# Optimization experiments

Hardware: AMD Instinct MI355X
Metric: run time of the kernel (lower is better)

Reference implementation:

```python
import jax, jax.numpy as jnp
import numpy as np

N_NODES = 50000
N_EDGES = 600000
IN_DIM = 128
HID = 128
OUT_DIM = 2


def _init_linear(key, out_dim, in_dim):
    scale = 1.0 / np.sqrt(in_dim)
    return jax.random.uniform(key, (out_dim, in_dim), jnp.float32, -scale, scale)


def setup_inputs() -> dict:
    key = jax.random.key(0)
    ks = jax.random.split(key, 12)
    x = jax.random.normal(ks[0], (N_NODES, IN_DIM), jnp.float32)
    edge_index = jax.random.randint(ks[1], (2, N_EDGES), 0, N_NODES, jnp.int64)
    dims = [(HID, IN_DIM), (HID, HID), (OUT_DIM, HID)]
    inp = {"x": x, "edge_index": edge_index}
    for i, (o, d) in enumerate(dims):
        inp[f"Wl{i}"] = _init_linear(ks[2 + 3 * i], o, d)      # lin_l: applied to aggregated neighbors
        inp[f"Wr{i}"] = _init_linear(ks[3 + 3 * i], o, d)      # lin_r: applied to root (self) features
        inp[f"b{i}"] = jnp.zeros((o,), jnp.float32)            # bias of lin_l
    return inp


def _sage_conv(x, src, dst, Wl, Wr, b):
    # mean-aggregate source features onto target nodes, then linear transform
    msgs = x[src]                                              # [E, d] gather
    agg = jax.ops.segment_sum(msgs, dst, num_segments=N_NODES)
    cnt = jax.ops.segment_sum(jnp.ones((src.shape[0], 1), x.dtype), dst,
                              num_segments=N_NODES)
    agg = agg / jnp.maximum(cnt, 1.0)                          # mean over in-edges
    return agg @ Wl.T + b + x @ Wr.T


def reference(x, edge_index, Wl0, Wr0, b0, Wl1, Wr1, b1, Wl2, Wr2, b2):
    src, dst = edge_index[0], edge_index[1]
    # eval mode: dropout is identity
    h = jax.nn.relu(_sage_conv(x, src, dst, Wl0, Wr0, b0))
    h = jax.nn.relu(_sage_conv(h, src, dst, Wl1, Wr1, b1))
    return _sage_conv(h, src, dst, Wl2, Wr2, b2)
```

## Files before the change

kernel.cpp:

```cpp
#include <hip/hip_runtime.h>
#include <hip/hip_bf16.h>

#define N_NODES 50000
#define N_EDGES 600000
#define DIM 128
#define CAP 64

typedef short bf16x8 __attribute__((ext_vector_type(8)));
typedef float f32x4 __attribute__((ext_vector_type(4)));

__device__ __forceinline__ ushort f2b(float f) {
    __hip_bfloat16 h = __float2bfloat16(f);
    return *reinterpret_cast<ushort*>(&h);
}
__device__ __forceinline__ float b2f_lo(unsigned u) { return __uint_as_float(u << 16); }
__device__ __forceinline__ float b2f_hi(unsigned u) { return __uint_as_float(u & 0xffff0000u); }

static constexpr size_t alignup(size_t x) { return (x + 255) & ~size_t(255); }
static constexpr size_t OFF_FLAG = 0;
static constexpr size_t OFF_CNT  = 256;
static constexpr size_t OFF_COL  = alignup(OFF_CNT + sizeof(unsigned) * N_NODES);
static constexpr size_t OFF_XBF  = alignup(OFF_COL + sizeof(int) * (size_t)N_NODES * CAP);
static constexpr size_t OFF_AGG  = alignup(OFF_XBF + sizeof(ushort) * N_NODES * DIM);
static constexpr size_t OFF_H1   = alignup(OFF_AGG + sizeof(ushort) * N_NODES * DIM);
static constexpr size_t OFF_Z    = alignup(OFF_H1 + sizeof(ushort) * N_NODES * DIM);
static constexpr size_t OFF_RT   = alignup(OFF_Z + sizeof(float) * 2 * N_NODES);
static constexpr size_t OFF_WL0  = alignup(OFF_RT + sizeof(float) * 2 * N_NODES);
static constexpr size_t OFF_WR0  = alignup(OFF_WL0 + sizeof(ushort) * DIM * DIM);
static constexpr size_t OFF_WL1  = alignup(OFF_WR0 + sizeof(ushort) * DIM * DIM);
static constexpr size_t OFF_WR1  = alignup(OFF_WL1 + sizeof(ushort) * DIM * DIM);

__global__ __launch_bounds__(256) void prep_k(const int* __restrict__ ei,
                                              const float* __restrict__ x,
                                              const float* __restrict__ wa, const float* __restrict__ wb,
                                              const float* __restrict__ wc, const float* __restrict__ wd,
                                              unsigned* __restrict__ flag,
                                              unsigned* __restrict__ cnt,
                                              ushort* __restrict__ xbf,
                                              ushort* __restrict__ oa, ushort* __restrict__ ob,
                                              ushort* __restrict__ oc, ushort* __restrict__ od) {
    const int bid = blockIdx.x, t = threadIdx.x;
    if (bid < 6250) {
        const int i = bid * 256 + t;
        float4 v = reinterpret_cast<const float4*>(x)[i];
        ushort4 o;
        o.x = f2b(v.x); o.y = f2b(v.y); o.z = f2b(v.z); o.w = f2b(v.w);
        reinterpret_cast<ushort4*>(xbf)[i] = o;
        if (i < N_NODES) cnt[i] = 0u;
        if (bid == 0) {
            __shared__ unsigned any;
            if (t == 0) any = 0u;
            __syncthreads();
            unsigned hv = 0;
#pragma unroll
            for (int j = 0; j < 4; ++j) hv |= (unsigned)ei[2 * (t * 4 + j) + 1];
            if (hv) atomicOr(&any, 1u);
            __syncthreads();
            if (t == 0) *flag = any;
        }
    } else {
        const int wb_i = bid - 6250;
        const int w = wb_i >> 4;
        const float* src = (w == 0) ? wa : (w == 1) ? wb : (w == 2) ? wc : wd;
        ushort* dst      = (w == 0) ? oa : (w == 1) ? ob : (w == 2) ? oc : od;
        const int i = (wb_i & 15) * 256 + t;
        float4 v = reinterpret_cast<const float4*>(src)[i];
        ushort4 o;
        o.x = f2b(v.x); o.y = f2b(v.y); o.z = f2b(v.z); o.w = f2b(v.w);
        reinterpret_cast<ushort4*>(dst)[i] = o;
    }
}

__global__ void fillcsr_k(const int* __restrict__ ei, const unsigned* __restrict__ flag,
                          unsigned* __restrict__ cnt, int* __restrict__ col) {
    int e0 = (blockIdx.x * 256 + threadIdx.x) * 4;
    if (e0 >= N_EDGES) return;
    int s[4], d[4];
    if (*flag) {
        uint4 sv = *reinterpret_cast<const uint4*>(&ei[e0]);
        uint4 dv = *reinterpret_cast<const uint4*>(&ei[N_EDGES + e0]);
        s[0] = sv.x; s[1] = sv.y; s[2] = sv.z; s[3] = sv.w;
        d[0] = dv.x; d[1] = dv.y; d[2] = dv.z; d[3] = dv.w;
    } else {
        uint4 sa = *reinterpret_cast<const uint4*>(&ei[2 * e0]);
        uint4 sb = *reinterpret_cast<const uint4*>(&ei[2 * e0 + 4]);
        uint4 da = *reinterpret_cast<const uint4*>(&ei[2 * (N_EDGES + e0)]);
        uint4 db = *reinterpret_cast<const uint4*>(&ei[2 * (N_EDGES + e0) + 4]);
        s[0] = sa.x; s[1] = sa.z; s[2] = sb.x; s[3] = sb.z;
        d[0] = da.x; d[1] = da.z; d[2] = db.x; d[3] = db.z;
    }
#pragma unroll
    for (int i = 0; i < 4; ++i) {
        unsigned pos = atomicAdd(&cnt[d[i]], 1u);
        if (pos < CAP) col[(size_t)d[i] * CAP + pos] = s[i];
    }
}

__global__ __launch_bounds__(256) void agg_k(const ushort* __restrict__ h,
                                             const unsigned* __restrict__ cnt,
                                             const int* __restrict__ col,
                                             ushort* __restrict__ aggm) {
    const int g = threadIdx.x >> 4, lane = threadIdx.x & 15;
    const int node = blockIdx.x * 16 + g;
    if (node >= N_NODES) return;
    unsigned deg = cnt[node];
    if (deg > CAP) deg = CAP;
    const int* cp = &col[(size_t)node * CAP];
    float acc[8];
#pragma unroll
    for (int i = 0; i < 8; ++i) acc[i] = 0.f;
    const int co = lane * 8;
    unsigned e = 0;
    for (; e + 4 <= deg; e += 4) {
        const int s0 = cp[e], s1 = cp[e + 1], s2 = cp[e + 2], s3 = cp[e + 3];
        const uint4 v0 = *reinterpret_cast<const uint4*>(&h[(size_t)s0 * DIM + co]);
        const uint4 v1 = *reinterpret_cast<const uint4*>(&h[(size_t)s1 * DIM + co]);
        const uint4 v2 = *reinterpret_cast<const uint4*>(&h[(size_t)s2 * DIM + co]);
        const uint4 v3 = *reinterpret_cast<const uint4*>(&h[(size_t)s3 * DIM + co]);
        acc[0] += b2f_lo(v0.x) + b2f_lo(v1.x) + b2f_lo(v2.x) + b2f_lo(v3.x);
        acc[1] += b2f_hi(v0.x) + b2f_hi(v1.x) + b2f_hi(v2.x) + b2f_hi(v3.x);
        acc[2] += b2f_lo(v0.y) + b2f_lo(v1.y) + b2f_lo(v2.y) + b2f_lo(v3.y);
        acc[3] += b2f_hi(v0.y) + b2f_hi(v1.y) + b2f_hi(v2.y) + b2f_hi(v3.y);
        acc[4] += b2f_lo(v0.z) + b2f_lo(v1.z) + b2f_lo(v2.z) + b2f_lo(v3.z);
        acc[5] += b2f_hi(v0.z) + b2f_hi(v1.z) + b2f_hi(v2.z) + b2f_hi(v3.z);
        acc[6] += b2f_lo(v0.w) + b2f_lo(v1.w) + b2f_lo(v2.w) + b2f_lo(v3.w);
        acc[7] += b2f_hi(v0.w) + b2f_hi(v1.w) + b2f_hi(v2.w) + b2f_hi(v3.w);
    }
    for (; e < deg; ++e) {
        const int s = cp[e];
        const uint4 v = *reinterpret_cast<const uint4*>(&h[(size_t)s * DIM + co]);
        acc[0] += b2f_lo(v.x); acc[1] += b2f_hi(v.x);
        acc[2] += b2f_lo(v.y); acc[3] += b2f_hi(v.y);
        acc[4] += b2f_lo(v.z); acc[5] += b2f_hi(v.z);
        acc[6] += b2f_lo(v.w); acc[7] += b2f_hi(v.w);
    }
    const float inv = 1.0f / fmaxf((float)deg, 1.0f);
    uint4 o;
    o.x = (unsigned)f2b(acc[0] * inv) | ((unsigned)f2b(acc[1] * inv) << 16);
    o.y = (unsigned)f2b(acc[2] * inv) | ((unsigned)f2b(acc[3] * inv) << 16);
    o.z = (unsigned)f2b(acc[4] * inv) | ((unsigned)f2b(acc[5] * inv) << 16);
    o.w = (unsigned)f2b(acc[6] * inv) | ((unsigned)f2b(acc[7] * inv) << 16);
    *reinterpret_cast<uint4*>(&aggm[(size_t)node * DIM + co]) = o;
}

__global__ __launch_bounds__(256) void xform_mfma_k(const ushort* __restrict__ A0,
                                                    const ushort* __restrict__ A1,
                                                    const ushort* __restrict__ Wl,
                                                    const ushort* __restrict__ Wr,
                                                    const float*  __restrict__ bias,
                                                    ushort* __restrict__ hout) {
    __shared__ ushort Ws[128 * 136];
    const int t    = threadIdx.x;
    const int wave = t >> 6;
    const int l    = t & 63;
    const int l16  = l & 15;
    const int lk   = (l >> 4) * 8;
    const int node = blockIdx.x * 64 + wave * 16 + l16;
    const bool valid = node < N_NODES;

    const int wrow = t >> 1;
    const int wc0  = (t & 1) * 64;

    f32x4 acc[8];
#pragma unroll
    for (int i = 0; i < 8; ++i) acc[i] = (f32x4){0.f, 0.f, 0.f, 0.f};

    const bf16x8 zfrag = (bf16x8){0, 0, 0, 0, 0, 0, 0, 0};

#pragma unroll
    for (int p = 0; p < 2; ++p) {
        const ushort* Asrc = p ? A1 : A0;
        const ushort* Wsrc = p ? Wr : Wl;

        bf16x8 bf[4];
#pragma unroll
        for (int ks = 0; ks < 4; ++ks)
            bf[ks] = valid
                ? *reinterpret_cast<const bf16x8*>(&Asrc[(size_t)node * DIM + ks * 32 + lk])
                : zfrag;

        __syncthreads();
        {
            const uint4* src = reinterpret_cast<const uint4*>(&Wsrc[(size_t)wrow * DIM + wc0]);
            uint4* dst = reinterpret_cast<uint4*>(&Ws[wrow * 136 + wc0]);
#pragma unroll
            for (int i = 0; i < 8; ++i) dst[i] = src[i];
        }
        __syncthreads();

#pragma unroll
        for (int ks = 0; ks < 4; ++ks) {
            const int kb = ks * 32;
#pragma unroll
            for (int ot = 0; ot < 8; ++ot) {
                const bf16x8 afrag = *reinterpret_cast<const bf16x8*>(
                    &Ws[(ot * 16 + l16) * 136 + kb + lk]);
                acc[ot] = __builtin_amdgcn_mfma_f32_16x16x32_bf16(afrag, bf[ks], acc[ot], 0, 0, 0);
            }
        }
    }

    if (!valid) return;
    const int orow = (l >> 4) * 4;
#pragma unroll
    for (int ot = 0; ot < 8; ++ot) {
        const float4 b4 = *reinterpret_cast<const float4*>(&bias[ot * 16 + orow]);
        float r0 = fmaxf(acc[ot][0] + b4.x, 0.f);
        float r1 = fmaxf(acc[ot][1] + b4.y, 0.f);
        float r2 = fmaxf(acc[ot][2] + b4.z, 0.f);
        float r3 = fmaxf(acc[ot][3] + b4.w, 0.f);
        ushort4 s;
        s.x = f2b(r0); s.y = f2b(r1); s.z = f2b(r2); s.w = f2b(r3);
        *reinterpret_cast<ushort4*>(&hout[(size_t)node * DIM + ot * 16 + orow]) = s;
    }
}

__global__ __launch_bounds__(256) void xform_final_k(const ushort* __restrict__ A0,
                                                     const ushort* __restrict__ A1,
                                                     const ushort* __restrict__ Wl,
                                                     const ushort* __restrict__ Wr,
                                                     const float*  __restrict__ bias,
                                                     const float*  __restrict__ Wl2,
                                                     const float*  __restrict__ Wr2,
                                                     const float*  __restrict__ b2,
                                                     float* __restrict__ z,
                                                     float* __restrict__ rt) {
    __shared__ ushort Ws[128 * 136];
    __shared__ float wl2s[256], wr2s[256];
    const int t    = threadIdx.x;
    const int wave = t >> 6;
    const int l    = t & 63;
    const int l16  = l & 15;
    const int lk   = (l >> 4) * 8;
    const int node = blockIdx.x * 64 + wave * 16 + l16;
    const bool valid = node < N_NODES;

    const int wrow = t >> 1;
    const int wc0  = (t & 1) * 64;

    wl2s[t] = Wl2[t];
    wr2s[t] = Wr2[t];

    f32x4 acc[8];
#pragma unroll
    for (int i = 0; i < 8; ++i) acc[i] = (f32x4){0.f, 0.f, 0.f, 0.f};

    const bf16x8 zfrag = (bf16x8){0, 0, 0, 0, 0, 0, 0, 0};

#pragma unroll
    for (int p = 0; p < 2; ++p) {
        const ushort* Asrc = p ? A1 : A0;
        const ushort* Wsrc = p ? Wr : Wl;

        bf16x8 bf[4];
#pragma unroll
        for (int ks = 0; ks < 4; ++ks)
            bf[ks] = valid
                ? *reinterpret_cast<const bf16x8*>(&Asrc[(size_t)node * DIM + ks * 32 + lk])
                : zfrag;

        __syncthreads();
        {
            const uint4* src = reinterpret_cast<const uint4*>(&Wsrc[(size_t)wrow * DIM + wc0]);
            uint4* dst = reinterpret_cast<uint4*>(&Ws[wrow * 136 + wc0]);
#pragma unroll
            for (int i = 0; i < 8; ++i) dst[i] = src[i];
        }
        __syncthreads();

#pragma unroll
        for (int ks = 0; ks < 4; ++ks) {
            const int kb = ks * 32;
#pragma unroll
            for (int ot = 0; ot < 8; ++ot) {
                const bf16x8 afrag = *reinterpret_cast<const bf16x8*>(
                    &Ws[(ot * 16 + l16) * 136 + kb + lk]);
                acc[ot] = __builtin_amdgcn_mfma_f32_16x16x32_bf16(afrag, bf[ks], acc[ot], 0, 0, 0);
            }
        }
    }

    const int orow = (l >> 4) * 4;
    float z0 = 0.f, z1 = 0.f, r0s = 0.f, r1s = 0.f;
#pragma unroll
    for (int ot = 0; ot < 8; ++ot) {
        const int o = ot * 16 + orow;
        const float4 b4 = *reinterpret_cast<const float4*>(&bias[o]);
        const float h0 = fmaxf(acc[ot][0] + b4.x, 0.f);
        const float h1v = fmaxf(acc[ot][1] + b4.y, 0.f);
        const float h2v = fmaxf(acc[ot][2] + b4.z, 0.f);
        const float h3 = fmaxf(acc[ot][3] + b4.w, 0.f);
        z0  += h0 * wl2s[o] + h1v * wl2s[o + 1] + h2v * wl2s[o + 2] + h3 * wl2s[o + 3];
        z1  += h0 * wl2s[128 + o] + h1v * wl2s[128 + o + 1] + h2v * wl2s[128 + o + 2] + h3 * wl2s[128 + o + 3];
        r0s += h0 * wr2s[o] + h1v * wr2s[o + 1] + h2v * wr2s[o + 2] + h3 * wr2s[o + 3];
        r1s += h0 * wr2s[128 + o] + h1v * wr2s[128 + o + 1] + h2v * wr2s[128 + o + 2] + h3 * wr2s[128 + o + 3];
    }
    z0  += __shfl_xor(z0, 16);  z0  += __shfl_xor(z0, 32);
    z1  += __shfl_xor(z1, 16);  z1  += __shfl_xor(z1, 32);
    r0s += __shfl_xor(r0s, 16); r0s += __shfl_xor(r0s, 32);
    r1s += __shfl_xor(r1s, 16); r1s += __shfl_xor(r1s, 32);
    if ((l >> 4) == 0 && valid) {
        float2 zv = {z0, z1};
        float2 rv = {r0s + b2[0], r1s + b2[1]};
        *reinterpret_cast<float2*>(&z[(size_t)node * 2])  = zv;
        *reinterpret_cast<float2*>(&rt[(size_t)node * 2]) = rv;
    }
}

__global__ __launch_bounds__(256) void outgather_k(const float* __restrict__ z,
                                                   const float* __restrict__ rt,
                                                   const unsigned* __restrict__ cnt,
                                                   const int* __restrict__ col,
                                                   float* __restrict__ out) {
    const int g = threadIdx.x >> 3, lane = threadIdx.x & 7;
    const int node = blockIdx.x * 32 + g;
    if (node >= N_NODES) return;
    unsigned deg = cnt[node];
    if (deg > CAP) deg = CAP;
    const int* cp = &col[(size_t)node * CAP];
    float s0 = 0.f, s1 = 0.f;
    for (unsigned e = lane; e < deg; e += 8) {
        const int s = cp[e];
        const float2 v = *reinterpret_cast<const float2*>(&z[(size_t)s * 2]);
        s0 += v.x; s1 += v.y;
    }
#pragma unroll
    for (int m = 1; m < 8; m <<= 1) {
        s0 += __shfl_xor(s0, m);
        s1 += __shfl_xor(s1, m);
    }
    if (lane == 0) {
        const float inv = 1.0f / fmaxf((float)deg, 1.0f);
        const float2 rv = *reinterpret_cast<const float2*>(&rt[(size_t)node * 2]);
        float2 o = {s0 * inv + rv.x, s1 * inv + rv.y};
        *reinterpret_cast<float2*>(&out[(size_t)node * 2]) = o;
    }
}

extern "C" void kernel_launch(void* const* d_in, const int* in_sizes, int n_in,
                              void* d_out, int out_size, void* d_ws, size_t ws_size,
                              hipStream_t stream) {
    const float* x   = (const float*)d_in[0];
    const int*   ei  = (const int*)d_in[1];
    const float* Wl0 = (const float*)d_in[2];
    const float* Wr0 = (const float*)d_in[3];
    const float* b0  = (const float*)d_in[4];
    const float* Wl1 = (const float*)d_in[5];
    const float* Wr1 = (const float*)d_in[6];
    const float* b1  = (const float*)d_in[7];
    const float* Wl2 = (const float*)d_in[8];
    const float* Wr2 = (const float*)d_in[9];
    const float* b2  = (const float*)d_in[10];

    char* ws = (char*)d_ws;
    unsigned* flag = (unsigned*)(ws + OFF_FLAG);
    unsigned* cnt  = (unsigned*)(ws + OFF_CNT);
    int*      col  = (int*)(ws + OFF_COL);
    ushort*   xbf  = (ushort*)(ws + OFF_XBF);
    ushort*   aggm = (ushort*)(ws + OFF_AGG);
    ushort*   h1   = (ushort*)(ws + OFF_H1);
    float*    zbuf = (float*)(ws + OFF_Z);
    float*    rtb  = (float*)(ws + OFF_RT);
    ushort*   wl0b = (ushort*)(ws + OFF_WL0);
    ushort*   wr0b = (ushort*)(ws + OFF_WR0);
    ushort*   wl1b = (ushort*)(ws + OFF_WL1);
    ushort*   wr1b = (ushort*)(ws + OFF_WR1);
    float*    out  = (float*)d_out;

    prep_k<<<6250 + 64, 256, 0, stream>>>(ei, x, Wl0, Wr0, Wl1, Wr1,
                                          flag, cnt, xbf, wl0b, wr0b, wl1b, wr1b);
    fillcsr_k<<<(N_EDGES / 4 + 255) / 256, 256, 0, stream>>>(ei, flag, cnt, col);

    agg_k<<<(N_NODES + 15) / 16, 256, 0, stream>>>(xbf, cnt, col, aggm);
    xform_mfma_k<<<(N_NODES + 63) / 64, 256, 0, stream>>>(aggm, xbf, wl0b, wr0b, b0, h1);
    agg_k<<<(N_NODES + 15) / 16, 256, 0, stream>>>(h1, cnt, col, aggm);
    xform_final_k<<<(N_NODES + 63) / 64, 256, 0, stream>>>(aggm, h1, wl1b, wr1b, b1,
                                                           Wl2, Wr2, b2, zbuf, rtb);
    outgather_k<<<(N_NODES + 31) / 32, 256, 0, stream>>>(zbuf, rtb, cnt, col, out);
}
```

Measured before the change: 133.7 us.

## Assign one wave per node in aggregation and two node tiles per wave in MFMA transforms

The aggregation kernel now maps a full 64-lane wave to each node, with each lane loading one 32-bit pair of bf16 values instead of 16 lanes loading 16-byte vectors. This spreads the gather over more lanes and shortens per-node dependency chains, at the cost of narrower loads. Both MFMA transform kernels now process two 16-node tiles per wave, so each shared-memory weight fragment feeds two MFMAs and the block count is halved. That raises register use for the accumulators and may lower occupancy.

```diff
diff --git a/kernel.cpp b/kernel.cpp
--- a/kernel.cpp
+++ b/kernel.cpp
@@ -100,47 +100,31 @@
                                              const unsigned* __restrict__ cnt,
                                              const int* __restrict__ col,
                                              ushort* __restrict__ aggm) {
-    const int g = threadIdx.x >> 4, lane = threadIdx.x & 15;
-    const int node = blockIdx.x * 16 + g;
-    if (node >= N_NODES) return;
+    const int wave = threadIdx.x >> 6;
+    const int l    = threadIdx.x & 63;
+    const int node = blockIdx.x * 4 + wave;
     unsigned deg = cnt[node];
     if (deg > CAP) deg = CAP;
     const int* cp = &col[(size_t)node * CAP];
-    float acc[8];
-#pragma unroll
-    for (int i = 0; i < 8; ++i) acc[i] = 0.f;
-    const int co = lane * 8;
+    const int co = l * 2;
+    float a0 = 0.f, a1 = 0.f;
     unsigned e = 0;
     for (; e + 4 <= deg; e += 4) {
         const int s0 = cp[e], s1 = cp[e + 1], s2 = cp[e + 2], s3 = cp[e + 3];
-        const uint4 v0 = *reinterpret_cast<const uint4*>(&h[(size_t)s0 * DIM + co]);
-        const uint4 v1 = *reinterpret_cast<const uint4*>(&h[(size_t)s1 * DIM + co]);
-        const uint4 v2 = *reinterpret_cast<const uint4*>(&h[(size_t)s2 * DIM + co]);
-        const uint4 v3 = *reinterpret_cast<const uint4*>(&h[(size_t)s3 * DIM + co]);
-        acc[0] += b2f_lo(v0.x) + b2f_lo(v1.x) + b2f_lo(v2.x) + b2f_lo(v3.x);
-        acc[1] += b2f_hi(v0.x) + b2f_hi(v1.x) + b2f_hi(v2.x) + b2f_hi(v3.x);
-        acc[2] += b2f_lo(v0.y) + b2f_lo(v1.y) + b2f_lo(v2.y) + b2f_lo(v3.y);
-        acc[3] += b2f_hi(v0.y) + b2f_hi(v1.y) + b2f_hi(v2.y) + b2f_hi(v3.y);
-        acc[4] += b2f_lo(v0.z) + b2f_lo(v1.z) + b2f_lo(v2.z) + b2f_lo(v3.z);
-        acc[5] += b2f_hi(v0.z) + b2f_hi(v1.z) + b2f_hi(v2.z) + b2f_hi(v3.z);
-        acc[6] += b2f_lo(v0.w) + b2f_lo(v1.w) + b2f_lo(v2.w) + b2f_lo(v3.w);
-        acc[7] += b2f_hi(v0.w) + b2f_hi(v1.w) + b2f_hi(v2.w) + b2f_hi(v3.w);
+        const unsigned v0 = *reinterpret_cast<const unsigned*>(&h[(size_t)s0 * DIM + co]);
+        const unsigned v1 = *reinterpret_cast<const unsigned*>(&h[(size_t)s1 * DIM + co]);
+        const unsigned v2 = *reinterpret_cast<const unsigned*>(&h[(size_t)s2 * DIM + co]);
+        const unsigned v3 = *reinterpret_cast<const unsigned*>(&h[(size_t)s3 * DIM + co]);
+        a0 += b2f_lo(v0) + b2f_lo(v1) + b2f_lo(v2) + b2f_lo(v3);
+        a1 += b2f_hi(v0) + b2f_hi(v1) + b2f_hi(v2) + b2f_hi(v3);
     }
     for (; e < deg; ++e) {
-        const int s = cp[e];
-        const uint4 v = *reinterpret_cast<const uint4*>(&h[(size_t)s * DIM + co]);
-        acc[0] += b2f_lo(v.x); acc[1] += b2f_hi(v.x);
-        acc[2] += b2f_lo(v.y); acc[3] += b2f_hi(v.y);
-        acc[4] += b2f_lo(v.z); acc[5] += b2f_hi(v.z);
-        acc[6] += b2f_lo(v.w); acc[7] += b2f_hi(v.w);
+        const unsigned v = *reinterpret_cast<const unsigned*>(&h[(size_t)cp[e] * DIM + co]);
+        a0 += b2f_lo(v); a1 += b2f_hi(v);
     }
     const float inv = 1.0f / fmaxf((float)deg, 1.0f);
-    uint4 o;
-    o.x = (unsigned)f2b(acc[0] * inv) | ((unsigned)f2b(acc[1] * inv) << 16);
-    o.y = (unsigned)f2b(acc[2] * inv) | ((unsigned)f2b(acc[3] * inv) << 16);
-    o.z = (unsigned)f2b(acc[4] * inv) | ((unsigned)f2b(acc[5] * inv) << 16);
-    o.w = (unsigned)f2b(acc[6] * inv) | ((unsigned)f2b(acc[7] * inv) << 16);
-    *reinterpret_cast<uint4*>(&aggm[(size_t)node * DIM + co]) = o;
+    const unsigned o = (unsigned)f2b(a0 * inv) | ((unsigned)f2b(a1 * inv) << 16);
+    *reinterpret_cast<unsigned*>(&aggm[(size_t)node * DIM + co]) = o;
 }
 
 __global__ __launch_bounds__(256) void xform_mfma_k(const ushort* __restrict__ A0,
@@ -155,15 +139,18 @@
     const int l    = t & 63;
     const int l16  = l & 15;
     const int lk   = (l >> 4) * 8;
-    const int node = blockIdx.x * 64 + wave * 16 + l16;
-    const bool valid = node < N_NODES;
+    const int n0   = blockIdx.x * 128 + wave * 32 + l16;
+    const int n1   = n0 + 16;
+    const bool v0 = n0 < N_NODES, v1 = n1 < N_NODES;
 
     const int wrow = t >> 1;
     const int wc0  = (t & 1) * 64;
 
-    f32x4 acc[8];
-#pragma unroll
-    for (int i = 0; i < 8; ++i) acc[i] = (f32x4){0.f, 0.f, 0.f, 0.f};
+    f32x4 acc[2][8];
+#pragma unroll
+    for (int b = 0; b < 2; ++b)
+#pragma unroll
+        for (int i = 0; i < 8; ++i) acc[b][i] = (f32x4){0.f, 0.f, 0.f, 0.f};
 
     const bf16x8 zfrag = (bf16x8){0, 0, 0, 0, 0, 0, 0, 0};
 
@@ -172,12 +159,12 @@
         const ushort* Asrc = p ? A1 : A0;
         const ushort* Wsrc = p ? Wr : Wl;
 
-        bf16x8 bf[4];
-#pragma unroll
-        for (int ks = 0; ks < 4; ++ks)
-            bf[ks] = valid
-                ? *reinterpret_cast<const bf16x8*>(&Asrc[(size_t)node * DIM + ks * 32 + lk])
-                : zfrag;
+        bf16x8 bf0[4], bf1[4];
+#pragma unroll
+        for (int ks = 0; ks < 4; ++ks) {
+            bf0[ks] = v0 ? *reinterpret_cast<const bf16x8*>(&Asrc[(size_t)n0 * DIM + ks * 32 + lk]) : zfrag;
+            bf1[ks] = v1 ? *reinterpret_cast<const bf16x8*>(&Asrc[(size_t)n1 * DIM + ks * 32 + lk]) : zfrag;
+        }
 
         __syncthreads();
         {
@@ -195,23 +182,28 @@
             for (int ot = 0; ot < 8; ++ot) {
                 const bf16x8 afrag = *reinterpret_cast<const bf16x8*>(
                     &Ws[(ot * 16 + l16) * 136 + kb + lk]);
-                acc[ot] = __builtin_amdgcn_mfma_f32_16x16x32_bf16(afrag, bf[ks], acc[ot], 0, 0, 0);
+                acc[0][ot] = __builtin_amdgcn_mfma_f32_16x16x32_bf16(afrag, bf0[ks], acc[0][ot], 0, 0, 0);
+                acc[1][ot] = __builtin_amdgcn_mfma_f32_16x16x32_bf16(afrag, bf1[ks], acc[1][ot], 0, 0, 0);
             }
         }
     }
 
-    if (!valid) return;
     const int orow = (l >> 4) * 4;
 #pragma unroll
-    for (int ot = 0; ot < 8; ++ot) {
-        const float4 b4 = *reinterpret_cast<const float4*>(&bias[ot * 16 + orow]);
-        float r0 = fmaxf(acc[ot][0] + b4.x, 0.f);
-        float r1 = fmaxf(acc[ot][1] + b4.y, 0.f);
-        float r2 = fmaxf(acc[ot][2] + b4.z, 0.f);
-        float r3 = fmaxf(acc[ot][3] + b4.w, 0.f);
-        ushort4 s;
-        s.x = f2b(r0); s.y = f2b(r1); s.z = f2b(r2); s.w = f2b(r3);
-        *reinterpret_cast<ushort4*>(&hout[(size_t)node * DIM + ot * 16 + orow]) = s;
+    for (int b = 0; b < 2; ++b) {
+        const int node = n0 + b * 16;
+        if (node >= N_NODES) continue;
+#pragma unroll
+        for (int ot = 0; ot < 8; ++ot) {
+            const float4 b4 = *reinterpret_cast<const float4*>(&bias[ot * 16 + orow]);
+            float r0 = fmaxf(acc[b][ot][0] + b4.x, 0.f);
+            float r1 = fmaxf(acc[b][ot][1] + b4.y, 0.f);
+            float r2 = fmaxf(acc[b][ot][2] + b4.z, 0.f);
+            float r3 = fmaxf(acc[b][ot][3] + b4.w, 0.f);
+            ushort4 s;
+            s.x = f2b(r0); s.y = f2b(r1); s.z = f2b(r2); s.w = f2b(r3);
+            *reinterpret_cast<ushort4*>(&hout[(size_t)node * DIM + ot * 16 + orow]) = s;
+        }
     }
 }
 
@@ -232,8 +224,9 @@
     const int l    = t & 63;
     const int l16  = l & 15;
     const int lk   = (l >> 4) * 8;
-    const int node = blockIdx.x * 64 + wave * 16 + l16;
-    const bool valid = node < N_NODES;
+    const int n0   = blockIdx.x * 128 + wave * 32 + l16;
+    const int n1   = n0 + 16;
+    const bool v0 = n0 < N_NODES, v1 = n1 < N_NODES;
 
     const int wrow = t >> 1;
     const int wc0  = (t & 1) * 64;
@@ -241,9 +234,11 @@
     wl2s[t] = Wl2[t];
     wr2s[t] = Wr2[t];
 
-    f32x4 acc[8];
-#pragma unroll
-    for (int i = 0; i < 8; ++i) acc[i] = (f32x4){0.f, 0.f, 0.f, 0.f};
+    f32x4 acc[2][8];
+#pragma unroll
+    for (int b = 0; b < 2; ++b)
+#pragma unroll
+        for (int i = 0; i < 8; ++i) acc[b][i] = (f32x4){0.f, 0.f, 0.f, 0.f};
 
     const bf16x8 zfrag = (bf16x8){0, 0, 0, 0, 0, 0, 0, 0};
 
@@ -252,12 +247,12 @@
         const ushort* Asrc = p ? A1 : A0;
         const ushort* Wsrc = p ? Wr : Wl;
 
-        bf16x8 bf[4];
-#pragma unroll
-        for (int ks = 0; ks < 4; ++ks)
-            bf[ks] = valid
-                ? *reinterpret_cast<const bf16x8*>(&Asrc[(size_t)node * DIM + ks * 32 + lk])
-                : zfrag;
+        bf16x8 bf0[4], bf1[4];
+#pragma unroll
+        for (int ks = 0; ks < 4; ++ks) {
+            bf0[ks] = v0 ? *reinterpret_cast<const bf16x8*>(&Asrc[(size_t)n0 * DIM + ks * 32 + lk]) : zfrag;
+            bf1[ks] = v1 ? *reinterpret_cast<const bf16x8*>(&Asrc[(size_t)n1 * DIM + ks * 32 + lk]) : zfrag;
+        }
 
         __syncthreads();
         {
@@ -275,35 +270,40 @@
             for (int ot = 0; ot < 8; ++ot) {
                 const bf16x8 afrag = *reinterpret_cast<const bf16x8*>(
                     &Ws[(ot * 16 + l16) * 136 + kb + lk]);
-                acc[ot] = __builtin_amdgcn_mfma_f32_16x16x32_bf16(afrag, bf[ks], acc[ot], 0, 0, 0);
+                acc[0][ot] = __builtin_amdgcn_mfma_f32_16x16x32_bf16(afrag, bf0[ks], acc[0][ot], 0, 0, 0);
+                acc[1][ot] = __builtin_amdgcn_mfma_f32_16x16x32_bf16(afrag, bf1[ks], acc[1][ot], 0, 0, 0);
             }
         }
     }
 
     const int orow = (l >> 4) * 4;
-    float z0 = 0.f, z1 = 0.f, r0s = 0.f, r1s = 0.f;
-#pragma unroll
-    for (int ot = 0; ot < 8; ++ot) {
-        const int o = ot * 16 + orow;
-        const float4 b4 = *reinterpret_cast<const float4*>(&bias[o]);
-        const float h0 = fmaxf(acc[ot][0] + b4.x, 0.f);
-        const float h1v = fmaxf(acc[ot][1] + b4.y, 0.f);
-        const float h2v = fmaxf(acc[ot][2] + b4.z, 0.f);
-        const float h3 = fmaxf(acc[ot][3] + b4.w, 0.f);
-        z0  += h0 * wl2s[o] + h1v * wl2s[o + 1] + h2v * wl2s[o + 2] + h3 * wl2s[o + 3];
-        z1  += h0 * wl2s[128 + o] + h1v * wl2s[128 + o + 1] + h2v * wl2s[128 + o + 2] + h3 * wl2s[128 + o + 3];
-        r0s += h0 * wr2s[o] + h1v * wr2s[o + 1] + h2v * wr2s[o + 2] + h3 * wr2s[o + 3];
-        r1s += h0 * wr2s[128 + o] + h1v * wr2s[128 + o + 1] + h2v * wr2s[128 + o + 2] + h3 * wr2s[128 + o + 3];
-    }
-    z0  += __shfl_xor(z0, 16);  z0  += __shfl_xor(z0, 32);
-    z1  += __shfl_xor(z1, 16);  z1  += __shfl_xor(z1, 32);
-    r0s += __shfl_xor(r0s, 16); r0s += __shfl_xor(r0s, 32);
-    r1s += __shfl_xor(r1s, 16); r1s += __shfl_xor(r1s, 32);
-    if ((l >> 4) == 0 && valid) {
-        float2 zv = {z0, z1};
-        float2 rv = {r0s + b2[0], r1s + b2[1]};
-        *reinterpret_cast<float2*>(&z[(size_t)node * 2])  = zv;
-        *reinterpret_cast<float2*>(&rt[(size_t)node * 2]) = rv;
+#pragma unroll
+    for (int b = 0; b < 2; ++b) {
+        float z0 = 0.f, z1 = 0.f, r0s = 0.f, r1s = 0.f;
+#pragma unroll
+        for (int ot = 0; ot < 8; ++ot) {
+            const int o = ot * 16 + orow;
+            const float4 b4 = *reinterpret_cast<const float4*>(&bias[o]);
+            const float h0 = fmaxf(acc[b][ot][0] + b4.x, 0.f);
+            const float h1v = fmaxf(acc[b][ot][1] + b4.y, 0.f);
+            const float h2v = fmaxf(acc[b][ot][2] + b4.z, 0.f);
+            const float h3 = fmaxf(acc[b][ot][3] + b4.w, 0.f);
+            z0  += h0 * wl2s[o] + h1v * wl2s[o + 1] + h2v * wl2s[o + 2] + h3 * wl2s[o + 3];
+            z1  += h0 * wl2s[128 + o] + h1v * wl2s[128 + o + 1] + h2v * wl2s[128 + o + 2] + h3 * wl2s[128 + o + 3];
+            r0s += h0 * wr2s[o] + h1v * wr2s[o + 1] + h2v * wr2s[o + 2] + h3 * wr2s[o + 3];
+            r1s += h0 * wr2s[128 + o] + h1v * wr2s[128 + o + 1] + h2v * wr2s[128 + o + 2] + h3 * wr2s[128 + o + 3];
+        }
+        z0  += __shfl_xor(z0, 16);  z0  += __shfl_xor(z0, 32);
+        z1  += __shfl_xor(z1, 16);  z1  += __shfl_xor(z1, 32);
+        r0s += __shfl_xor(r0s, 16); r0s += __shfl_xor(r0s, 32);
+        r1s += __shfl_xor(r1s, 16); r1s += __shfl_xor(r1s, 32);
+        const int node = n0 + b * 16;
+        if ((l >> 4) == 0 && node < N_NODES) {
+            float2 zv = {z0, z1};
+            float2 rv = {r0s + b2[0], r1s + b2[1]};
+            *reinterpret_cast<float2*>(&z[(size_t)node * 2])  = zv;
+            *reinterpret_cast<float2*>(&rt[(size_t)node * 2]) = rv;
+        }
     }
 }
 
@@ -371,10 +371,10 @@
                                           flag, cnt, xbf, wl0b, wr0b, wl1b, wr1b);
     fillcsr_k<<<(N_EDGES / 4 + 255) / 256, 256, 0, stream>>>(ei, flag, cnt, col);
 
-    agg_k<<<(N_NODES + 15) / 16, 256, 0, stream>>>(xbf, cnt, col, aggm);
-    xform_mfma_k<<<(N_NODES + 63) / 64, 256, 0, stream>>>(aggm, xbf, wl0b, wr0b, b0, h1);
-    agg_k<<<(N_NODES + 15) / 16, 256, 0, stream>>>(h1, cnt, col, aggm);
-    xform_final_k<<<(N_NODES + 63) / 64, 256, 0, stream>>>(aggm, h1, wl1b, wr1b, b1,
-                                                           Wl2, Wr2, b2, zbuf, rtb);
+    agg_k<<<N_NODES / 4, 256, 0, stream>>>(xbf, cnt, col, aggm);
+    xform_mfma_k<<<(N_NODES + 127) / 128, 256, 0, stream>>>(aggm, xbf, wl0b, wr0b, b0, h1);
+    agg_k<<<N_NODES / 4, 256, 0, stream>>>(h1, cnt, col, aggm);
+    xform_final_k<<<(N_NODES + 127) / 128, 256, 0, stream>>>(aggm, h1, wl1b, wr1b, b1,
+                                                             Wl2, Wr2, b2, zbuf, rtb);
     outgather_k<<<(N_NODES + 31) / 32, 256, 0, stream>>>(zbuf, rtb, cnt, col, out);
 }
```

Result: slower. 143.1 us (+7.0%).
